# Kernel optimization log

Hardware: AMD Instinct MI355X
Metric: run time of the kernel (lower is better)

The kernel has to match this reference:

```python
import jax, jax.numpy as jnp
import numpy as np
from jax.scipy.linalg import solve_triangular

B, S, HIDDEN = 2, 2048, 2048
HK, HV, DK, DV = 16, 32, 128, 128
KCONV = 4
CHUNK = 64
EPS = 1e-6
KEY_DIM = HK * DK        # 2048
VALUE_DIM = HV * DV      # 4096
CONV_DIM = 2 * KEY_DIM + VALUE_DIM  # 8192


def setup_inputs() -> dict:
    key = jax.random.key(0)
    ks = jax.random.split(key, 8)
    s = lambda n: 1.0 / np.sqrt(n)
    return {
        "hidden_states": jax.random.normal(ks[0], (B, S, HIDDEN), jnp.float32),
        "W_qkvz": jax.random.normal(ks[1], (HIDDEN, 2 * KEY_DIM + 2 * VALUE_DIM), jnp.float32) * s(HIDDEN),
        "W_ba": jax.random.normal(ks[2], (HIDDEN, 2 * HV), jnp.float32) * s(HIDDEN),
        "conv_weight": jax.random.normal(ks[3], (CONV_DIM, KCONV), jnp.float32) * s(KCONV),
        "dt_bias": jnp.ones((HV,), jnp.float32),
        "A_log": jax.random.normal(ks[4], (HV,), jnp.float32) * 0.1,
        "norm_weight": jnp.ones((DV,), jnp.float32),
        "W_out": jax.random.normal(ks[5], (VALUE_DIM, HIDDEN), jnp.float32) * s(VALUE_DIM),
    }


def _chunk_gated_delta_rule(q, k, v, g, beta):
    # q,k: [B,H,S,DK] (l2-normalized); v: [B,H,S,DV]; g,beta: [B,H,S]
    Bq, H, Sq, Dk = q.shape
    N = Sq // CHUNK
    q = q * (Dk ** -0.5)
    rs = lambda x: x.reshape(Bq, H, N, CHUNK, x.shape[-1])
    q, k, v = rs(q), rs(k), rs(v)
    g = g.reshape(Bq, H, N, CHUNK)
    beta = beta.reshape(Bq, H, N, CHUNK)
    gc = jnp.cumsum(g, axis=-1)  # within-chunk cumulative log-decay
    tri = jnp.tril(jnp.ones((CHUNK, CHUNK), bool))
    tri_s = jnp.tril(jnp.ones((CHUNK, CHUNK), bool), -1)
    decay = jnp.where(tri, jnp.exp(gc[..., :, None] - gc[..., None, :]), 0.0)
    k_beta = k * beta[..., None]
    v_beta = v * beta[..., None]
    # strictly-lower within-chunk interaction matrix; T = (I + A)^{-1} (fwd substitution)
    A = jnp.where(tri_s, jnp.einsum('bhncd,bhnkd->bhnck', k_beta, k) * decay, 0.0)
    eye = jnp.eye(CHUNK, dtype=q.dtype)
    T = solve_triangular(eye + A, jnp.broadcast_to(eye, A.shape), lower=True)
    v_adj = T @ v_beta                                    # [B,H,N,C,DV]
    k_cumdecay = T @ (k_beta * jnp.exp(gc)[..., None])    # [B,H,N,C,DK]
    attn_local = jnp.where(tri, jnp.einsum('bhncd,bhnkd->bhnck', q, k) * decay, 0.0)

    def step(state, xs):
        q_i, k_i, vadj_i, kcd_i, g_i, attn_i = xs          # per-chunk slices [B,H,C,*]
        v_new = vadj_i - kcd_i @ state                     # [B,H,C,DV]
        o = (q_i * jnp.exp(g_i)[..., None]) @ state + attn_i @ v_new
        g_last = g_i[..., -1]                              # [B,H]
        decayed_k = k_i * jnp.exp(g_last[..., None] - g_i)[..., None]
        state = state * jnp.exp(g_last)[..., None, None] + jnp.einsum('bhcd,bhcv->bhdv', decayed_k, v_new)
        return state, o

    mv = lambda x: jnp.moveaxis(x, 2, 0)
    state0 = jnp.zeros((Bq, H, Dk, v.shape[-1]), q.dtype)
    _, o = jax.lax.scan(step, state0, (mv(q), mv(k), mv(v_adj), mv(k_cumdecay), mv(gc), mv(attn_local)))
    return jnp.moveaxis(o, 0, 2).reshape(Bq, H, Sq, -1)


def reference(hidden_states, W_qkvz, W_ba, conv_weight, dt_bias, A_log, norm_weight, W_out):
    B_, S_, _ = hidden_states.shape
    # fused QKVZ / BA projections, contiguous layout [q|k|v|z], [b|a]
    qkvz = hidden_states @ W_qkvz
    q, k, v, z = jnp.split(qkvz, [KEY_DIM, 2 * KEY_DIM, 2 * KEY_DIM + VALUE_DIM], axis=-1)
    b, a = jnp.split(hidden_states @ W_ba, 2, axis=-1)
    beta = jax.nn.sigmoid(b)                                   # [B,S,HV]
    g = -jnp.exp(A_log) * jax.nn.softplus(a + dt_bias)         # [B,S,HV]
    # causal depthwise conv over [q|k|v] channels + silu
    mixed = jnp.concatenate([q, k, v], axis=-1)                # [B,S,CONV_DIM]
    pad = jnp.pad(mixed, ((0, 0), (KCONV - 1, 0), (0, 0)))
    conv = sum(pad[:, j:j + S_, :] * conv_weight[:, j] for j in range(KCONV))
    conv = jax.nn.silu(conv)
    q, k, v = jnp.split(conv, [KEY_DIM, 2 * KEY_DIM], axis=-1)
    q = q.reshape(B_, S_, HK, DK)
    k = k.reshape(B_, S_, HK, DK)
    v = v.reshape(B_, S_, HV, DV)
    l2n = lambda x: x * jax.lax.rsqrt(jnp.sum(x * x, -1, keepdims=True) + 1e-6)
    q, k = l2n(q), l2n(k)
    rep = HV // HK  # each qk head serves rep consecutive v heads
    q = jnp.repeat(q, rep, axis=2)
    k = jnp.repeat(k, rep, axis=2)
    tr = lambda x: jnp.swapaxes(x, 1, 2)                       # -> [B,H,S,D]
    o = _chunk_gated_delta_rule(tr(q), tr(k), tr(v), jnp.swapaxes(g, 1, 2), jnp.swapaxes(beta, 1, 2))
    o = jnp.swapaxes(o, 1, 2)                                  # [B,S,HV,DV]
    # gated RMSNorm (norm before gate): rmsnorm(o) * w * silu(z)
    z = z.reshape(B_, S_, HV, DV)
    o = o * jax.lax.rsqrt(jnp.mean(o * o, -1, keepdims=True) + EPS)
    o = o * norm_weight * jax.nn.silu(z)
    return o.reshape(B_, S_, VALUE_DIM) @ W_out
```

## Files before the change

### kernel.cpp

```cpp
#include <hip/hip_runtime.h>
#include <hip/hip_bf16.h>


typedef short bf16x8 __attribute__((ext_vector_type(8)));
typedef float f32x4  __attribute__((ext_vector_type(4)));

#define MFMA_BF16(a,b,c) __builtin_amdgcn_mfma_f32_16x16x32_bf16((a),(b),(c),0,0,0)
#define GLD16(g,l) __builtin_amdgcn_global_load_lds((const __attribute__((address_space(1))) void*)(g), (__attribute__((address_space(3))) void*)(l), 16, 0, 0)

__device__ __forceinline__ unsigned short f2bf(float x){
  union { float f; unsigned u; } v; v.f = x;
  return (unsigned short)((v.u + 0x7fffu + ((v.u >> 16) & 1u)) >> 16);
}
__device__ __forceinline__ float bf2f(unsigned short h){
  union { unsigned u; float f; } v; v.u = ((unsigned)h) << 16; return v.f;
}
__device__ __forceinline__ unsigned long long pack4bf(float a, float b, float c, float d){
  return (unsigned long long)f2bf(a) | ((unsigned long long)f2bf(b) << 16)
       | ((unsigned long long)f2bf(c) << 32) | ((unsigned long long)f2bf(d) << 48);
}

__global__ __launch_bounds__(256) void cast_bf16_kernel(
    const float* __restrict__ in, unsigned short* __restrict__ out, int n)
{
  int i = (blockIdx.x * 256 + threadIdx.x) * 4;
  if (i >= n) return;
  float4 v = *(const float4*)(in + i);
  *(unsigned long long*)(out + i) = pack4bf(v.x, v.y, v.z, v.w);
}

__global__ __launch_bounds__(256) void transpose_cast_kernel(
    const float* __restrict__ W, unsigned short* __restrict__ WT, int R, int C)
{
  __shared__ __attribute__((aligned(16))) float tile[32][33];
  int c0 = blockIdx.x * 32, r0 = blockIdx.y * 32;
  int tx = threadIdx.x & 31, ty = threadIdx.x >> 5;
  #pragma unroll
  for (int i = 0; i < 32; i += 8)
    tile[ty + i][tx] = W[(size_t)(r0 + ty + i) * C + c0 + tx];
  __syncthreads();
  #pragma unroll
  for (int i = 0; i < 32; i += 8)
    WT[(size_t)(c0 + ty + i) * R + r0 + tx] = f2bf(tile[tx][ty + i]);
}

template<bool BF16OUT>
__global__ __launch_bounds__(256) void gemm_bt(
    const unsigned short* __restrict__ A,
    const unsigned short* __restrict__ B,
    void* __restrict__ Cv, int M, int N, int K)
{
  __shared__ __attribute__((aligned(16))) unsigned short Abuf[128 * 32];
  __shared__ __attribute__((aligned(16))) unsigned short Bbuf[128 * 32];
  const int tid  = threadIdx.x;
  const int wave = tid >> 6, lane = tid & 63;
  const int quad = lane >> 4, l16 = lane & 15;
  const int m0 = blockIdx.x * 128, n0 = blockIdx.y * 128;
  const int wm = (wave & 1) * 64, wn = (wave >> 1) * 64;

  f32x4 acc[4][4];
  #pragma unroll
  for (int a = 0; a < 4; ++a)
    #pragma unroll
    for (int b = 0; b < 4; ++b)
      #pragma unroll
      for (int r = 0; r < 4; ++r) acc[a][b][r] = 0.f;

  const int nkt = K >> 5;
  for (int kt = 0; kt < nkt; ++kt) {
    const int k0 = kt << 5;
    __syncthreads();
    #pragma unroll
    for (int c = 0; c < 2; ++c) {
      int p   = (wave * 2 + c) * 64 + lane;
      int m   = p >> 2;
      int gch = (p & 3) ^ ((m >> 2) & 3);
      GLD16(A + (size_t)(m0 + m) * K + k0 + gch * 8, Abuf + (wave * 2 + c) * 512);
      GLD16(B + (size_t)(n0 + m) * K + k0 + gch * 8, Bbuf + (wave * 2 + c) * 512);
    }
    __syncthreads();
    bf16x8 af[4], bfv[4];
    #pragma unroll
    for (int mt = 0; mt < 4; ++mt) {
      int m = wm + mt * 16 + l16;
      af[mt] = *(const bf16x8*)(Abuf + (m * 4 + (quad ^ ((m >> 2) & 3))) * 8);
    }
    #pragma unroll
    for (int nt = 0; nt < 4; ++nt) {
      int n = wn + nt * 16 + l16;
      bfv[nt] = *(const bf16x8*)(Bbuf + (n * 4 + (quad ^ ((n >> 2) & 3))) * 8);
    }
    #pragma unroll
    for (int mt = 0; mt < 4; ++mt)
      #pragma unroll
      for (int nt = 0; nt < 4; ++nt)
        acc[mt][nt] = MFMA_BF16(af[mt], bfv[nt], acc[mt][nt]);
  }
  #pragma unroll
  for (int mt = 0; mt < 4; ++mt) {
    #pragma unroll
    for (int nt = 0; nt < 4; ++nt) {
      int row = m0 + wm + mt * 16 + quad * 4;
      int col = n0 + wn + nt * 16 + l16;
      #pragma unroll
      for (int r = 0; r < 4; ++r) {
        if (BF16OUT)
          ((unsigned short*)Cv)[(size_t)(row + r) * N + col] = f2bf(acc[mt][nt][r]);
        else
          ((float*)Cv)[(size_t)(row + r) * N + col] = acc[mt][nt][r];
      }
    }
  }
}

__global__ __launch_bounds__(512, 2) void gemm256_bt(
    const unsigned short* __restrict__ A,
    const unsigned short* __restrict__ B,
    unsigned short* __restrict__ C, int M, int N, int K)
{
  __shared__ __attribute__((aligned(16))) unsigned short lds[65536];

  const int tid  = threadIdx.x;
  const int wave = tid >> 6, lane = tid & 63;
  const int quad = lane >> 4, l16 = lane & 15;
  const int wm8 = (wave >> 2) << 3;
  const int wn4 = (wave & 3) << 2;

  int wg = blockIdx.x;
  if ((gridDim.x & 7) == 0) {
    int qq = (int)gridDim.x >> 3;
    wg = (wg & 7) * qq + (wg >> 3);
  }
  const int tm = M >> 8;
  const int m0 = (wg % tm) << 8;
  const int n0 = (wg / tm) << 8;

  const int rd_off = ((l16 << 6) + (quad << 4)) ^ ((l16 >> 3) << 5);

  const int st_off = wave << 9;
  const int src_c  = ((wave & 1) << 5) + (((lane & 3) << 3) ^ ((lane >> 5) << 4));
  const unsigned short* Asrc = A + (size_t)(m0 + ((wave >> 1) << 4) + (lane >> 2)) * K + src_c;
  const unsigned short* Bsrc = B + (size_t)(n0 + ((wave >> 1) << 4) + (lane >> 2)) * K + src_c;

  const int NT = K >> 6;

#define STA(t, qi) GLD16(Asrc + (size_t)(qi) * 64 * K + (t) * 64, \
                         lds + (((t) & 1) << 15) + st_off + ((qi) << 12))
#define STB(t, qi) GLD16(Bsrc + (size_t)(qi) * 64 * K + (t) * 64, \
                         lds + (((t) & 1) << 15) + 16384 + st_off + ((qi) << 12))
#define RDA(dst, P)                                                            \
  _Pragma("unroll")                                                            \
  for (int j = 0; j < 2; ++j)                                                  \
    _Pragma("unroll")                                                          \
    for (int kb = 0; kb < 2; ++kb)                                             \
      dst[j][kb] = *(const bf16x8*)(Ar + ((((wm8 + 2 * (P) + j) << 1) | kb) << 10) + rd_off);
#define MMA(P, AF)                                                             \
  __builtin_amdgcn_s_setprio(1);                                               \
  _Pragma("unroll")                                                            \
  for (int j = 0; j < 2; ++j)                                                  \
    _Pragma("unroll")                                                          \
    for (int nf = 0; nf < 4; ++nf)                                             \
      _Pragma("unroll")                                                        \
      for (int kb = 0; kb < 2; ++kb)                                           \
        acc[2 * (P) + j][nf] = MFMA_BF16(AF[j][kb], b8[nf][kb], acc[2 * (P) + j][nf]); \
  __builtin_amdgcn_s_setprio(0);
#define LGKM4  asm volatile("s_waitcnt lgkmcnt(4)" ::: "memory");              \
               __builtin_amdgcn_sched_barrier(0)
#define LGKM0  asm volatile("s_waitcnt lgkmcnt(0)" ::: "memory");              \
               __builtin_amdgcn_sched_barrier(0)

  f32x4 acc[8][4];
  #pragma unroll
  for (int a = 0; a < 8; ++a)
    #pragma unroll
    for (int b = 0; b < 4; ++b)
      #pragma unroll
      for (int r = 0; r < 4; ++r) acc[a][b][r] = 0.f;

  STB(0, 0); STB(0, 1); STB(0, 2); STB(0, 3);
  STA(0, 0); STA(0, 1); STA(0, 2); STA(0, 3);
  if (NT > 1) {
    STB(1, 0); STB(1, 1); STB(1, 2); STB(1, 3); STA(1, 0); STA(1, 2);
    asm volatile("s_waitcnt vmcnt(6)" ::: "memory");
  } else {
    asm volatile("s_waitcnt vmcnt(0)" ::: "memory");
  }
  __builtin_amdgcn_s_barrier();

  for (int u = 0; u < NT; ++u) {
    const char* Ar = (const char*)lds + ((u & 1) << 16);
    const char* Br = Ar + 32768;
    bf16x8 b8[4][2], aA[2][2], aB[2][2];
    #pragma unroll
    for (int nf = 0; nf < 4; ++nf)
      #pragma unroll
      for (int kb = 0; kb < 2; ++kb)
        b8[nf][kb] = *(const bf16x8*)(Br + ((((wn4 + nf) << 1) | kb) << 10) + rd_off);
    RDA(aA, 0);
    __builtin_amdgcn_sched_barrier(0);

    RDA(aB, 1);
    if (u + 1 < NT) { STA(u + 1, 1); STA(u + 1, 3); }
    __builtin_amdgcn_s_barrier();
    LGKM4;
    MMA(0, aA);
    __builtin_amdgcn_s_barrier();

    RDA(aA, 2);
    if (u + 2 < NT) { STB(u + 2, 0); STB(u + 2, 1); }
    __builtin_amdgcn_s_barrier();
    LGKM4;
    MMA(1, aB);
    __builtin_amdgcn_s_barrier();

    RDA(aB, 3);
    if (u + 2 < NT) { STB(u + 2, 2); STA(u + 2, 0); }
    __builtin_amdgcn_s_barrier();
    LGKM4;
    MMA(2, aA);
    __builtin_amdgcn_s_barrier();

    if (u + 2 < NT) { STB(u + 2, 3); STA(u + 2, 2); }
    __builtin_amdgcn_s_barrier();
    LGKM0;
    MMA(3, aB);
    if (u + 2 < NT) asm volatile("s_waitcnt vmcnt(6)" ::: "memory");
    else            asm volatile("s_waitcnt vmcnt(0)" ::: "memory");
    __builtin_amdgcn_s_barrier();
  }
#undef RDA
#undef MMA
#undef LGKM4
#undef LGKM0
#undef STA
#undef STB

  #pragma unroll
  for (int mt = 0; mt < 8; ++mt) {
    int row = m0 + ((wave >> 2) << 7) + mt * 16 + (quad << 2);
    #pragma unroll
    for (int nf = 0; nf < 4; ++nf) {
      int col = n0 + ((wave & 3) << 6) + nf * 16 + l16;
      #pragma unroll
      for (int r = 0; r < 4; ++r)
        C[(size_t)(row + r) * N + col] = f2bf(acc[mt][nf][r]);
    }
  }
}

__global__ __launch_bounds__(256) void ba_kernel(
    const float* __restrict__ H, const float* __restrict__ Wba,
    const float* __restrict__ dtb, const float* __restrict__ Alog,
    float* __restrict__ bbuf, float* __restrict__ gbuf)
{
  int t = threadIdx.x;
  int col = t & 63, wv = t >> 6;
  int m0 = blockIdx.x * 16 + wv * 4;
  const float* h0 = H + (size_t)m0 * 2048;
  float a0 = 0.f, a1 = 0.f, a2 = 0.f, a3 = 0.f;
  for (int k = 0; k < 2048; ++k) {
    float w = Wba[k * 64 + col];
    a0 += h0[k]        * w;
    a1 += h0[2048 + k] * w;
    a2 += h0[4096 + k] * w;
    a3 += h0[6144 + k] * w;
  }
  float accv[4] = {a0, a1, a2, a3};
  #pragma unroll
  for (int r = 0; r < 4; ++r) {
    int m = m0 + r;
    int b = m >> 11, s = m & 2047;
    float acc = accv[r];
    if (col < 32) {
      bbuf[((size_t)(b * 32 + col)) * 2048 + s] = 1.f / (1.f + __expf(-acc));
    } else {
      int hh = col - 32;
      float x  = acc + dtb[hh];
      float sp = (x > 20.f) ? x : log1pf(__expf(x));
      gbuf[((size_t)(b * 32 + hh)) * 2048 + s] = -__expf(Alog[hh]) * sp;
    }
  }
}

__global__ __launch_bounds__(128) void conv_kernel(
    const unsigned short* __restrict__ qkvz, const float* __restrict__ cw,
    unsigned short* __restrict__ qn, unsigned short* __restrict__ kn,
    unsigned short* __restrict__ vb)
{
  int s_base = blockIdx.x * 4;
  int head   = blockIdx.y;
  int d      = threadIdx.x;
  int col    = head * 128 + d;
  int s_loc  = s_base & 2047;

  float vin[7];
  #pragma unroll
  for (int t = 0; t < 7; ++t) {
    int sp = s_loc + t - 3;
    vin[t] = (sp >= 0) ? bf2f(qkvz[(size_t)(s_base + t - 3) * 12288 + col]) : 0.f;
  }
  float w0 = cw[col*4], w1 = cw[col*4+1], w2 = cw[col*4+2], w3 = cw[col*4+3];
  float y[4];
  #pragma unroll
  for (int u = 0; u < 4; ++u) {
    float acc = vin[u]*w0 + vin[u+1]*w1 + vin[u+2]*w2 + vin[u+3]*w3;
    y[u] = acc / (1.f + __expf(-acc));
  }
  if (head < 32) {
    __shared__ float red[2][4];
    int wv = threadIdx.x >> 6;
    #pragma unroll
    for (int u = 0; u < 4; ++u) {
      float ss = y[u] * y[u];
      #pragma unroll
      for (int off = 32; off; off >>= 1) ss += __shfl_down(ss, off);
      if ((threadIdx.x & 63) == 0) red[wv][u] = ss;
    }
    __syncthreads();
    #pragma unroll
    for (int u = 0; u < 4; ++u) {
      float r = rsqrtf(red[0][u] + red[1][u] + 1e-6f);
      if (head < 16)
        qn[((size_t)(s_base + u) * 16 + head) * 128 + d] = f2bf(y[u] * r * 0.08838834764831845f);
      else
        kn[((size_t)(s_base + u) * 16 + (head - 16)) * 128 + d] = f2bf(y[u] * r);
    }
  } else {
    #pragma unroll
    for (int u = 0; u < 4; ++u)
      vb[((size_t)(s_base + u) * 32 + (head - 32)) * 128 + d] = f2bf(y[u]);
  }
}

__global__ __launch_bounds__(256) void chunk_kernel(
    const unsigned short* __restrict__ qnb, const unsigned short* __restrict__ knb,
    const unsigned short* __restrict__ vbb,
    const float* __restrict__ gbuf, const float* __restrict__ bbuf,
    unsigned short* __restrict__ attnb, unsigned short* __restrict__ vadjb,
    unsigned short* __restrict__ kcdn, unsigned short* __restrict__ qgb,
    unsigned short* __restrict__ kdT, float* __restrict__ egl)
{
  int cid = blockIdx.x;
  int n = cid & 31, h = (cid >> 5) & 31, b = cid >> 10;
  int h2 = h >> 1, s0 = n * 64;
  int gs0 = b * 2048 + s0;
  int tid = threadIdx.x, wave = tid >> 6, lane = tid & 63, quad = lane >> 4, l16 = lane & 15;

  __shared__ __attribute__((aligned(16))) unsigned short kS[64 * 136];
  __shared__ __attribute__((aligned(16))) float As[64 * 68];
  __shared__ float gcS[64], betaS[64];
  __shared__ float rsV[64], rsK[64], egq[64], egliS[64];

  if (tid < 64) {
    gcS[tid]   = gbuf[((size_t)(b * 32 + h)) * 2048 + s0 + tid];
    betaS[tid] = bbuf[((size_t)(b * 32 + h)) * 2048 + s0 + tid];
  }
  {
    int i = tid >> 2, seg = tid & 3;
    const bf16x8* kp = (const bf16x8*)(knb + ((size_t)(gs0 + i) * 16 + h2) * 128 + seg * 32);
    bf16x8* kd_ = (bf16x8*)(kS + i * 136 + seg * 32);
    #pragma unroll
    for (int u = 0; u < 4; ++u) kd_[u] = kp[u];
  }
  __syncthreads();
  if (tid == 0) {
    float run = 0.f;
    for (int i = 0; i < 64; ++i) { run += gcS[i]; gcS[i] = run; }
  }
  __syncthreads();

  if (tid < 64) {
    float gi = gcS[tid];
    rsV[tid]   = betaS[tid];
    rsK[tid]   = betaS[tid] * __expf(gi);
    egq[tid]   = __expf(gi);
    egliS[tid] = __expf(gcS[63] - gi);
    if (tid == 0) egl[cid] = __expf(gcS[63]);
  }

  {
    int arow = wave * 16 + l16;
    float bscale = betaS[arow];
    const unsigned short* qpg = qnb + ((size_t)(gs0 + arow) * 16 + h2) * 128;
    bf16x8 kbf[4], qf[4];
    #pragma unroll
    for (int ks = 0; ks < 4; ++ks) {
      bf16x8 kfr = *(const bf16x8*)(kS + arow * 136 + ks * 32 + quad * 8);
      bf16x8 t;
      #pragma unroll
      for (int e = 0; e < 8; ++e)
        t[e] = (short)f2bf(bf2f((unsigned short)kfr[e]) * bscale);
      kbf[ks] = t;
      qf[ks] = *(const bf16x8*)(qpg + ks * 32 + quad * 8);
    }
    #pragma unroll
    for (int jt = 0; jt < 4; ++jt) {
      f32x4 accA, accQ;
      #pragma unroll
      for (int r = 0; r < 4; ++r) { accA[r] = 0.f; accQ[r] = 0.f; }
      #pragma unroll
      for (int ks = 0; ks < 4; ++ks) {
        bf16x8 bfr = *(const bf16x8*)(kS + (jt * 16 + l16) * 136 + ks * 32 + quad * 8);
        accA = MFMA_BF16(kbf[ks], bfr, accA);
        accQ = MFMA_BF16(qf[ks],  bfr, accQ);
      }
      #pragma unroll
      for (int r = 0; r < 4; ++r) {
        int i = wave * 16 + quad * 4 + r;
        int j = jt * 16 + l16;
        float e = __expf(gcS[i] - gcS[j]);
        As[i * 68 + j] = (j < i) ? (accA[r] * e) : 0.f;
        attnb[(size_t)cid * 4096 + i * 64 + j] = (j <= i) ? f2bf(accQ[r] * e) : (unsigned short)0;
      }
    }
  }
  __syncthreads();

  {
    int c = tid;
    float x[64];
    if (c < 128) {
      const unsigned short* vp = vbb + ((size_t)gs0 * 32 + h) * 128 + c;
      #pragma unroll
      for (int i = 0; i < 64; ++i)
        x[i] = bf2f(vp[(size_t)i * 4096]) * rsV[i];
    } else {
      int ck = c - 128;
      #pragma unroll
      for (int i = 0; i < 64; ++i)
        x[i] = bf2f(kS[i * 136 + ck]) * rsK[i];
    }
    #pragma unroll
    for (int bi = 0; bi < 4; ++bi) {
      const int base = bi * 16;
      #pragma unroll
      for (int ii = 1; ii < 16; ++ii) {
        const int r = base + ii;
        const f32x4* ar = (const f32x4*)(As + r * 68 + base);
        float s = 0.f;
        #pragma unroll
        for (int g = 0; g < 4; ++g) {
          f32x4 a4 = ar[g];
          s += a4[0] * x[base + g*4] + a4[1] * x[base + g*4 + 1]
             + a4[2] * x[base + g*4 + 2] + a4[3] * x[base + g*4 + 3];
        }
        x[r] -= s;
      }
      #pragma unroll
      for (int r = base + 16; r < 64; ++r) {
        const f32x4* ar = (const f32x4*)(As + r * 68 + base);
        float s = 0.f;
        #pragma unroll
        for (int g = 0; g < 4; ++g) {
          f32x4 a4 = ar[g];
          s += a4[0] * x[base + g*4] + a4[1] * x[base + g*4 + 1]
             + a4[2] * x[base + g*4 + 2] + a4[3] * x[base + g*4 + 3];
        }
        x[r] -= s;
      }
    }
    if (c < 128) {
      unsigned short* vo = vadjb + (size_t)cid * 8192 + c;
      #pragma unroll
      for (int i = 0; i < 64; ++i) vo[i * 128] = f2bf(x[i]);
    } else {
      unsigned short* ko = kcdn + (size_t)cid * 8192 + (c - 128);
      #pragma unroll
      for (int i = 0; i < 64; ++i) ko[i * 128] = f2bf(-x[i]);
    }
  }

  {
    int i = tid >> 2, seg = tid & 3;
    float egli = egliS[i];
    float eqi  = egq[i];
    size_t base128 = (size_t)cid * 8192 + i * 128 + seg * 32;
    const unsigned short* qp = qnb + ((size_t)(gs0 + i) * 16 + h2) * 128 + seg * 32;
    #pragma unroll
    for (int u = 0; u < 32; u += 4) {
      *(unsigned long long*)(qgb + base128 + u) =
          pack4bf(bf2f(qp[u]) * eqi, bf2f(qp[u+1]) * eqi, bf2f(qp[u+2]) * eqi, bf2f(qp[u+3]) * eqi);
    }
    const unsigned short* kp = kS + i * 136 + seg * 32;
    unsigned short* kdo = kdT + (size_t)cid * 8192;
    #pragma unroll
    for (int u = 0; u < 32; ++u) {
      int d = seg * 32 + u;
      kdo[(size_t)d * 64 + i] = f2bf(bf2f(kp[u]) * egli);
    }
  }
}

__global__ __launch_bounds__(256) void scan_kernel(
    const unsigned short* __restrict__ qgb, const unsigned short* __restrict__ kcdn,
    const unsigned short* __restrict__ attnb, const unsigned short* __restrict__ kdT,
    const unsigned short* __restrict__ vadjb, const float* __restrict__ egl,
    unsigned short* __restrict__ obuf)
{
  int bh = blockIdx.x, dv0 = blockIdx.y * 32;
  int tid = threadIdx.x, w = tid >> 6, lane = tid & 63, quad = lane >> 4, l16 = lane & 15;
  __shared__ __attribute__((aligned(16))) unsigned short stT[32 * 136];
  __shared__ __attribute__((aligned(16))) unsigned short vnT[32 * 72];

  for (int idx = tid; idx < 32 * 136; idx += 256) stT[idx] = 0;
  f32x4 st[2][2];
  #pragma unroll
  for (int a = 0; a < 2; ++a)
    #pragma unroll
    for (int bq = 0; bq < 2; ++bq)
      #pragma unroll
      for (int r = 0; r < 4; ++r) st[a][bq][r] = 0.f;
  __syncthreads();

  for (int n = 0; n < 32; ++n) {
    size_t cid = (size_t)bh * 32 + n;
    const unsigned short* qgc = qgb  + cid * 8192;
    const unsigned short* kcc = kcdn + cid * 8192;
    const unsigned short* atc = attnb + cid * 4096;
    const unsigned short* kdc = kdT  + cid * 8192;
    const unsigned short* vac = vadjb + cid * 8192;
    float a = egl[cid];

    bf16x8 sf[2][4];
    #pragma unroll
    for (int ni = 0; ni < 2; ++ni)
      #pragma unroll
      for (int ks = 0; ks < 4; ++ks)
        sf[ni][ks] = *(const bf16x8*)(stT + (ni * 16 + l16) * 136 + ks * 32 + quad * 8);

    f32x4 vacc[2];
    #pragma unroll
    for (int ni = 0; ni < 2; ++ni)
      #pragma unroll
      for (int r = 0; r < 4; ++r)
        vacc[ni][r] = bf2f(vac[(size_t)(w * 16 + quad * 4 + r) * 128 + dv0 + ni * 16 + l16]);
    bf16x8 kf[4];
    #pragma unroll
    for (int ks = 0; ks < 4; ++ks)
      kf[ks] = *(const bf16x8*)(kcc + (size_t)(w * 16 + l16) * 128 + ks * 32 + quad * 8);
    #pragma unroll
    for (int ni = 0; ni < 2; ++ni)
      #pragma unroll
      for (int ks = 0; ks < 4; ++ks)
        vacc[ni] = MFMA_BF16(kf[ks], sf[ni][ks], vacc[ni]);

    f32x4 oacc[2];
    #pragma unroll
    for (int ni = 0; ni < 2; ++ni)
      #pragma unroll
      for (int r = 0; r < 4; ++r) oacc[ni][r] = 0.f;
    bf16x8 qf[4];
    #pragma unroll
    for (int ks = 0; ks < 4; ++ks)
      qf[ks] = *(const bf16x8*)(qgc + (size_t)(w * 16 + l16) * 128 + ks * 32 + quad * 8);
    #pragma unroll
    for (int ni = 0; ni < 2; ++ni)
      #pragma unroll
      for (int ks = 0; ks < 4; ++ks)
        oacc[ni] = MFMA_BF16(qf[ks], sf[ni][ks], oacc[ni]);

    #pragma unroll
    for (int ni = 0; ni < 2; ++ni)
      #pragma unroll
      for (int r = 0; r < 4; ++r)
        vnT[(ni * 16 + l16) * 72 + w * 16 + quad * 4 + r] = f2bf(vacc[ni][r]);
    __syncthreads();

    bf16x8 af2[2], vf[2][2];
    #pragma unroll
    for (int k2 = 0; k2 < 2; ++k2)
      af2[k2] = *(const bf16x8*)(atc + (size_t)(w * 16 + l16) * 64 + k2 * 32 + quad * 8);
    #pragma unroll
    for (int ni = 0; ni < 2; ++ni)
      #pragma unroll
      for (int k2 = 0; k2 < 2; ++k2)
        vf[ni][k2] = *(const bf16x8*)(vnT + (ni * 16 + l16) * 72 + k2 * 32 + quad * 8);
    #pragma unroll
    for (int ni = 0; ni < 2; ++ni)
      #pragma unroll
      for (int k2 = 0; k2 < 2; ++k2)
        oacc[ni] = MFMA_BF16(af2[k2], vf[ni][k2], oacc[ni]);
    unsigned short* op = obuf + ((size_t)bh * 2048 + n * 64) * 128;
    #pragma unroll
    for (int ni = 0; ni < 2; ++ni)
      #pragma unroll
      for (int r = 0; r < 4; ++r)
        op[(size_t)(w * 16 + quad * 4 + r) * 128 + dv0 + ni * 16 + l16] = f2bf(oacc[ni][r]);

    #pragma unroll
    for (int mi = 0; mi < 2; ++mi) {
      int mg = (w * 2 + mi) * 16;
      bf16x8 kdf[2];
      #pragma unroll
      for (int k2 = 0; k2 < 2; ++k2)
        kdf[k2] = *(const bf16x8*)(kdc + (size_t)(mg + l16) * 64 + k2 * 32 + quad * 8);
      #pragma unroll
      for (int ni = 0; ni < 2; ++ni) {
        f32x4 acc_;
        #pragma unroll
        for (int r = 0; r < 4; ++r) acc_[r] = a * st[mi][ni][r];
        #pragma unroll
        for (int k2 = 0; k2 < 2; ++k2)
          acc_ = MFMA_BF16(kdf[k2], vf[ni][k2], acc_);
        st[mi][ni] = acc_;
      }
    }
    #pragma unroll
    for (int mi = 0; mi < 2; ++mi)
      #pragma unroll
      for (int ni = 0; ni < 2; ++ni)
        #pragma unroll
        for (int r = 0; r < 4; ++r)
          stT[(ni * 16 + l16) * 136 + (w * 2 + mi) * 16 + quad * 4 + r] = f2bf(st[mi][ni][r]);
    __syncthreads();
  }
}

__global__ __launch_bounds__(256) void gate_kernel(
    const unsigned short* __restrict__ obuf, const unsigned short* __restrict__ qkvz,
    const float* __restrict__ nw, unsigned short* __restrict__ gated)
{
  int id = blockIdx.x * 4 + (threadIdx.x >> 6);
  int h = id & 31, bs = id >> 5;
  int b = bs >> 11, s = bs & 2047;
  int lane = threadIdx.x & 63;
  const unsigned short* op = obuf + (((size_t)(b * 32 + h)) * 2048 + s) * 128;
  const unsigned short* zp = qkvz + (size_t)bs * 12288 + 8192 + h * 128;
  float x0 = bf2f(op[lane]), x1 = bf2f(op[lane + 64]);
  float ss = x0 * x0 + x1 * x1;
  #pragma unroll
  for (int off = 32; off; off >>= 1) ss += __shfl_down(ss, off);
  ss = __shfl(ss, 0);
  float r = rsqrtf(ss * (1.f / 128.f) + 1e-6f);
  float z0 = bf2f(zp[lane]), z1 = bf2f(zp[lane + 64]);
  float g0 = z0 / (1.f + __expf(-z0)), g1 = z1 / (1.f + __expf(-z1));
  unsigned short* gp = gated + (size_t)bs * 4096 + h * 128;
  gp[lane]      = f2bf(x0 * r * nw[lane]      * g0);
  gp[lane + 64] = f2bf(x1 * r * nw[lane + 64] * g1);
}

extern "C" void kernel_launch(void* const* d_in, const int* in_sizes, int n_in,
                              void* d_out, int out_size, void* d_ws, size_t ws_size,
                              hipStream_t stream)
{
  const float* H     = (const float*)d_in[0];
  const float* Wqkvz = (const float*)d_in[1];
  const float* Wba   = (const float*)d_in[2];
  const float* cw    = (const float*)d_in[3];
  const float* dtb   = (const float*)d_in[4];
  const float* Alog  = (const float*)d_in[5];
  const float* nw    = (const float*)d_in[6];
  const float* Wout  = (const float*)d_in[7];
  float* out = (float*)d_out;

  const size_t U1 = 0;
  const size_t U2 = U1 + 67108864;
  const size_t U3 = U2 + 100663296;
  const size_t U4 = U3 + 16777216;
  const size_t U5 = U4 + 1048576;
  const size_t U6 = U5 + 151003136;
  const size_t NEED = U6 + 33554432;
  if (ws_size < NEED) return;

  char* base = (char*)d_ws;
  unsigned short* Hbf   = (unsigned short*)(base + U1);
  unsigned short* WqT   = (unsigned short*)(base + U1 + 16777216);
  unsigned short* qnb   = (unsigned short*)(base + U1);
  unsigned short* knb   = (unsigned short*)(base + U1 + 16777216);
  unsigned short* vbb   = (unsigned short*)(base + U1 + 33554432);
  unsigned short* qkvzb = (unsigned short*)(base + U2);
  unsigned short* WoT   = (unsigned short*)(base + U3);
  float*          bbuf  = (float*)(base + U4);
  float*          gbuf  = (float*)(base + U4 + 524288);
  unsigned short* attnb = (unsigned short*)(base + U5);
  unsigned short* vadjb = (unsigned short*)(base + U5 + 16777216);
  unsigned short* kcdn  = (unsigned short*)(base + U5 + 50331648);
  unsigned short* qgb   = (unsigned short*)(base + U5 + 83886080);
  unsigned short* kdTb  = (unsigned short*)(base + U5 + 117440512);
  float*          egl   = (float*)(base + U5 + 150994944);
  unsigned short* gated = (unsigned short*)(base + U5);
  unsigned short* obuf  = (unsigned short*)(base + U6);

  cast_bf16_kernel<<<8192, 256, 0, stream>>>(H, Hbf, 4096 * 2048);
  transpose_cast_kernel<<<dim3(12288 / 32, 2048 / 32), 256, 0, stream>>>(Wqkvz, WqT, 2048, 12288);
  transpose_cast_kernel<<<dim3(2048 / 32, 4096 / 32), 256, 0, stream>>>(Wout, WoT, 4096, 2048);
  gemm256_bt<<<768, 512, 0, stream>>>(Hbf, WqT, qkvzb, 4096, 12288, 2048);
  ba_kernel<<<256, 256, 0, stream>>>(H, Wba, dtb, Alog, bbuf, gbuf);
  conv_kernel<<<dim3(1024, 64), 128, 0, stream>>>(qkvzb, cw, qnb, knb, vbb);
  chunk_kernel<<<2048, 256, 0, stream>>>(qnb, knb, vbb, gbuf, bbuf, attnb, vadjb, kcdn, qgb, kdTb, egl);
  scan_kernel<<<dim3(64, 4), 256, 0, stream>>>(qgb, kcdn, attnb, kdTb, vadjb, egl, obuf);
  gate_kernel<<<32768, 256, 0, stream>>>(obuf, qkvzb, nw, gated);
  gemm_bt<false><<<dim3(32, 16), 256, 0, stream>>>(gated, WoT, out, 4096, 2048, 4096);
}
```

Measured before the change: 951.4 us.

## Replace output projection GEMM with pipelined 128x256 tile kernel

```diff
diff --git a/kernel.cpp b/kernel.cpp
--- a/kernel.cpp
+++ b/kernel.cpp
@@ -42,75 +42,6 @@
   #pragma unroll
   for (int i = 0; i < 32; i += 8)
     WT[(size_t)(c0 + ty + i) * R + r0 + tx] = f2bf(tile[tx][ty + i]);
-}
-
-template<bool BF16OUT>
-__global__ __launch_bounds__(256) void gemm_bt(
-    const unsigned short* __restrict__ A,
-    const unsigned short* __restrict__ B,
-    void* __restrict__ Cv, int M, int N, int K)
-{
-  __shared__ __attribute__((aligned(16))) unsigned short Abuf[128 * 32];
-  __shared__ __attribute__((aligned(16))) unsigned short Bbuf[128 * 32];
-  const int tid  = threadIdx.x;
-  const int wave = tid >> 6, lane = tid & 63;
-  const int quad = lane >> 4, l16 = lane & 15;
-  const int m0 = blockIdx.x * 128, n0 = blockIdx.y * 128;
-  const int wm = (wave & 1) * 64, wn = (wave >> 1) * 64;
-
-  f32x4 acc[4][4];
-  #pragma unroll
-  for (int a = 0; a < 4; ++a)
-    #pragma unroll
-    for (int b = 0; b < 4; ++b)
-      #pragma unroll
-      for (int r = 0; r < 4; ++r) acc[a][b][r] = 0.f;
-
-  const int nkt = K >> 5;
-  for (int kt = 0; kt < nkt; ++kt) {
-    const int k0 = kt << 5;
-    __syncthreads();
-    #pragma unroll
-    for (int c = 0; c < 2; ++c) {
-      int p   = (wave * 2 + c) * 64 + lane;
-      int m   = p >> 2;
-      int gch = (p & 3) ^ ((m >> 2) & 3);
-      GLD16(A + (size_t)(m0 + m) * K + k0 + gch * 8, Abuf + (wave * 2 + c) * 512);
-      GLD16(B + (size_t)(n0 + m) * K + k0 + gch * 8, Bbuf + (wave * 2 + c) * 512);
-    }
-    __syncthreads();
-    bf16x8 af[4], bfv[4];
-    #pragma unroll
-    for (int mt = 0; mt < 4; ++mt) {
-      int m = wm + mt * 16 + l16;
-      af[mt] = *(const bf16x8*)(Abuf + (m * 4 + (quad ^ ((m >> 2) & 3))) * 8);
-    }
-    #pragma unroll
-    for (int nt = 0; nt < 4; ++nt) {
-      int n = wn + nt * 16 + l16;
-      bfv[nt] = *(const bf16x8*)(Bbuf + (n * 4 + (quad ^ ((n >> 2) & 3))) * 8);
-    }
-    #pragma unroll
-    for (int mt = 0; mt < 4; ++mt)
-      #pragma unroll
-      for (int nt = 0; nt < 4; ++nt)
-        acc[mt][nt] = MFMA_BF16(af[mt], bfv[nt], acc[mt][nt]);
-  }
-  #pragma unroll
-  for (int mt = 0; mt < 4; ++mt) {
-    #pragma unroll
-    for (int nt = 0; nt < 4; ++nt) {
-      int row = m0 + wm + mt * 16 + quad * 4;
-      int col = n0 + wn + nt * 16 + l16;
-      #pragma unroll
-      for (int r = 0; r < 4; ++r) {
-        if (BF16OUT)
-          ((unsigned short*)Cv)[(size_t)(row + r) * N + col] = f2bf(acc[mt][nt][r]);
-        else
-          ((float*)Cv)[(size_t)(row + r) * N + col] = acc[mt][nt][r];
-      }
-    }
-  }
 }
 
 __global__ __launch_bounds__(512, 2) void gemm256_bt(
@@ -248,6 +179,128 @@
   }
 }
 
+__global__ __launch_bounds__(512, 2) void gemm128x256_bt(
+    const unsigned short* __restrict__ A,
+    const unsigned short* __restrict__ B,
+    float* __restrict__ C, int M, int N, int K)
+{
+  __shared__ __attribute__((aligned(16))) unsigned short lds[49152];
+
+  const int tid  = threadIdx.x;
+  const int wave = tid >> 6, lane = tid & 63;
+  const int quad = lane >> 4, l16 = lane & 15;
+  const int wm4 = (wave >> 2) << 2;
+  const int wn4 = (wave & 3) << 2;
+
+  int wg = blockIdx.x;
+  if ((gridDim.x & 7) == 0) {
+    int qq = (int)gridDim.x >> 3;
+    wg = (wg & 7) * qq + (wg >> 3);
+  }
+  const int tm = M >> 7;
+  const int m0 = (wg % tm) << 7;
+  const int n0 = (wg / tm) << 8;
+
+  const int rd_off = ((l16 << 6) + (quad << 4)) ^ ((l16 >> 3) << 5);
+  const int st_off = wave << 9;
+  const int src_c  = ((wave & 1) << 5) + (((lane & 3) << 3) ^ ((lane >> 5) << 4));
+  const unsigned short* Asrc = A + (size_t)(m0 + ((wave >> 1) << 4) + (lane >> 2)) * K + src_c;
+  const unsigned short* Bsrc = B + (size_t)(n0 + ((wave >> 1) << 4) + (lane >> 2)) * K + src_c;
+
+  const int NT = K >> 6;
+
+#define STA(t, qi) GLD16(Asrc + (size_t)(qi) * 64 * K + (t) * 64, \
+                         lds + (((t) & 1) * 24576) + st_off + ((qi) << 12))
+#define STB(t, qi) GLD16(Bsrc + (size_t)(qi) * 64 * K + (t) * 64, \
+                         lds + (((t) & 1) * 24576) + 8192 + st_off + ((qi) << 12))
+
+  f32x4 acc[4][4];
+  #pragma unroll
+  for (int a = 0; a < 4; ++a)
+    #pragma unroll
+    for (int b = 0; b < 4; ++b)
+      #pragma unroll
+      for (int r = 0; r < 4; ++r) acc[a][b][r] = 0.f;
+
+  STB(0, 0); STB(0, 1); STB(0, 2); STB(0, 3);
+  STA(0, 0); STA(0, 1);
+  if (NT > 1) {
+    STB(1, 0); STB(1, 1); STB(1, 2); STB(1, 3);
+    asm volatile("s_waitcnt vmcnt(4)" ::: "memory");
+  } else {
+    asm volatile("s_waitcnt vmcnt(0)" ::: "memory");
+  }
+  __builtin_amdgcn_s_barrier();
+
+  for (int u = 0; u < NT; ++u) {
+    const char* Ar = (const char*)lds + (u & 1) * 49152;
+    const char* Br = Ar + 16384;
+    bf16x8 b8[4][2], aA[2][2], aB[2][2];
+    #pragma unroll
+    for (int nf = 0; nf < 4; ++nf)
+      #pragma unroll
+      for (int kb = 0; kb < 2; ++kb)
+        b8[nf][kb] = *(const bf16x8*)(Br + ((((wn4 + nf) << 1) | kb) << 10) + rd_off);
+    #pragma unroll
+    for (int j = 0; j < 2; ++j)
+      #pragma unroll
+      for (int kb = 0; kb < 2; ++kb)
+        aA[j][kb] = *(const bf16x8*)(Ar + ((((wm4 + j) << 1) | kb) << 10) + rd_off);
+    __builtin_amdgcn_sched_barrier(0);
+
+    #pragma unroll
+    for (int j = 0; j < 2; ++j)
+      #pragma unroll
+      for (int kb = 0; kb < 2; ++kb)
+        aB[j][kb] = *(const bf16x8*)(Ar + ((((wm4 + 2 + j) << 1) | kb) << 10) + rd_off);
+    if (u + 1 < NT) { STA(u + 1, 0); STA(u + 1, 1); }
+    __builtin_amdgcn_s_barrier();
+    asm volatile("s_waitcnt lgkmcnt(4)" ::: "memory");
+    __builtin_amdgcn_sched_barrier(0);
+    __builtin_amdgcn_s_setprio(1);
+    #pragma unroll
+    for (int j = 0; j < 2; ++j)
+      #pragma unroll
+      for (int nf = 0; nf < 4; ++nf)
+        #pragma unroll
+        for (int kb = 0; kb < 2; ++kb)
+          acc[j][nf] = MFMA_BF16(aA[j][kb], b8[nf][kb], acc[j][nf]);
+    __builtin_amdgcn_s_setprio(0);
+    __builtin_amdgcn_s_barrier();
+
+    if (u + 2 < NT) { STB(u + 2, 0); STB(u + 2, 1); STB(u + 2, 2); STB(u + 2, 3); }
+    __builtin_amdgcn_s_barrier();
+    asm volatile("s_waitcnt lgkmcnt(0)" ::: "memory");
+    __builtin_amdgcn_sched_barrier(0);
+    __builtin_amdgcn_s_setprio(1);
+    #pragma unroll
+    for (int j = 0; j < 2; ++j)
+      #pragma unroll
+      for (int nf = 0; nf < 4; ++nf)
+        #pragma unroll
+        for (int kb = 0; kb < 2; ++kb)
+          acc[2 + j][nf] = MFMA_BF16(aB[j][kb], b8[nf][kb], acc[2 + j][nf]);
+    __builtin_amdgcn_s_setprio(0);
+    if (u + 2 < NT) asm volatile("s_waitcnt vmcnt(4)" ::: "memory");
+    else            asm volatile("s_waitcnt vmcnt(0)" ::: "memory");
+    __builtin_amdgcn_s_barrier();
+  }
+#undef STA
+#undef STB
+
+  #pragma unroll
+  for (int mt = 0; mt < 4; ++mt) {
+    int row = m0 + ((wave >> 2) << 6) + mt * 16 + (quad << 2);
+    #pragma unroll
+    for (int nf = 0; nf < 4; ++nf) {
+      int col = n0 + ((wave & 3) << 6) + nf * 16 + l16;
+      #pragma unroll
+      for (int r = 0; r < 4; ++r)
+        C[(size_t)(row + r) * N + col] = acc[mt][nf][r];
+    }
+  }
+}
+
 __global__ __launch_bounds__(256) void ba_kernel(
     const float* __restrict__ H, const float* __restrict__ Wba,
     const float* __restrict__ dtb, const float* __restrict__ Alog,
@@ -690,5 +743,5 @@
   chunk_kernel<<<2048, 256, 0, stream>>>(qnb, knb, vbb, gbuf, bbuf, attnb, vadjb, kcdn, qgb, kdTb, egl);
   scan_kernel<<<dim3(64, 4), 256, 0, stream>>>(qgb, kcdn, attnb, kdTb, vadjb, egl, obuf);
   gate_kernel<<<32768, 256, 0, stream>>>(obuf, qkvzb, nw, gated);
-  gemm_bt<false><<<dim3(32, 16), 256, 0, stream>>>(gated, WoT, out, 4096, 2048, 4096);
-}
+  gemm128x256_bt<<<256, 512, 0, stream>>>(gated, WoT, out, 4096, 2048, 4096);
+}
```

Result: faster. 904.7 us (-4.9%).
